# Performance work log

Hardware: AMD Instinct MI355X
Metric: run time of the kernel (lower is better)

## Reference

```python
import jax, jax.numpy as jnp
import numpy as np

B, S, HID, NH, D = 1, 2048, 4096, 32, 128
ROPE_THETA = 10000.0
EPS = 1e-5


def setup_inputs() -> dict:
    key = jax.random.key(0)
    ks = jax.random.split(key, 10)
    w_scale = 1.0 / np.sqrt(HID)
    return {
        "hidden_states": jax.random.normal(ks[0], (B, S, HID), jnp.float32),
        "position_ids": jnp.broadcast_to(jnp.arange(S, dtype=jnp.int32), (B, S)),
        "Wq": jax.random.normal(ks[1], (HID, HID), jnp.float32) * w_scale,
        "Wk": jax.random.normal(ks[2], (HID, HID), jnp.float32) * w_scale,
        "Wv": jax.random.normal(ks[3], (HID, HID), jnp.float32) * w_scale,
        "Wo": jax.random.normal(ks[4], (HID, HID), jnp.float32) * w_scale,
        "qn_w": 1.0 + 0.02 * jax.random.normal(ks[5], (1, D), jnp.float32),
        "qn_b": 0.02 * jax.random.normal(ks[6], (1, D), jnp.float32),
        "kn_w": 1.0 + 0.02 * jax.random.normal(ks[7], (1, D), jnp.float32),
        "kn_b": 0.02 * jax.random.normal(ks[8], (1, D), jnp.float32),
    }


def _head_layernorm(x, gamma, beta, n_heads):
    # x: [B, S, n_heads, D]; gamma/beta: [mp=1, D] repeat-interleaved to [n_heads, D]
    mu = jnp.mean(x, axis=-1, keepdims=True)
    var = jnp.mean(jnp.square(x - mu), axis=-1, keepdims=True)
    xn = (x - mu) * jax.lax.rsqrt(var + EPS)
    g = jnp.repeat(gamma, n_heads // gamma.shape[0], axis=0)  # [n_heads, D]
    b = jnp.repeat(beta, n_heads // beta.shape[0], axis=0)
    return xn * g + b


def _rope_cos_sin(position_ids, dim, dtype):
    inv_freq = 1.0 / (ROPE_THETA ** (jnp.arange(0, dim, 2, dtype=jnp.float32) / dim))
    freqs = position_ids.astype(jnp.float32)[..., None] * inv_freq  # [B, S, D/2]
    emb = jnp.concatenate([freqs, freqs], axis=-1)  # [B, S, D]
    # unsqueeze_dim=-2 -> broadcast over heads in BSND layout
    return jnp.cos(emb)[:, :, None, :].astype(dtype), jnp.sin(emb)[:, :, None, :].astype(dtype)


def _rotate_half(x):
    h = x.shape[-1] // 2
    return jnp.concatenate([-x[..., h:], x[..., :h]], axis=-1)


def reference(hidden_states, position_ids, Wq, Wk, Wv, Wo, qn_w, qn_b, kn_w, kn_b):
    b, s, hid = hidden_states.shape
    d = qn_w.shape[-1]
    nh = hid // d
    nkv = nh  # num_key_value_heads == num_heads for Chameleon-7B (groups=1)

    q = (hidden_states @ Wq).reshape(b, s, nh, d)
    k = (hidden_states @ Wk).reshape(b, s, nkv, d)
    v = (hidden_states @ Wv).reshape(b, s, nkv, d)

    q = _head_layernorm(q, qn_w, qn_b, nh)
    k = _head_layernorm(k, kn_w, kn_b, nkv)

    cos, sin = _rope_cos_sin(position_ids, d, q.dtype)
    q = q * cos + _rotate_half(q) * sin
    k = k * cos + _rotate_half(k) * sin

    scale = d ** -0.5
    scores = jnp.einsum("bqhd,bkhd->bhqk", q, k) * scale  # [B, H, S, S]
    causal = jnp.tril(jnp.ones((s, s), dtype=bool))
    scores = jnp.where(causal[None, None], scores, jnp.finfo(scores.dtype).min)
    probs = jax.nn.softmax(scores, axis=-1)
    attn = jnp.einsum("bhqk,bkhd->bqhd", probs, v).reshape(b, s, hid)
    return attn @ Wo
```

## Files before the change

kernel.cpp:

```cpp
#include <hip/hip_runtime.h>

#define S_LEN 2048
#define HID 4096
#define NH 32
#define HD 128
#define QKV_N 12288

typedef __attribute__((ext_vector_type(8))) short bf16x8;
typedef __attribute__((ext_vector_type(4))) float f32x4;

__device__ __forceinline__ unsigned short f2bf(float f) {
    unsigned int u = __float_as_uint(f);
    u += 0x7FFF + ((u >> 16) & 1);
    return (unsigned short)(u >> 16);
}
__device__ __forceinline__ float bf2f(unsigned short h) {
    return __uint_as_float(((unsigned int)h) << 16);
}

typedef __attribute__((address_space(1))) const void gconst_void;
typedef __attribute__((address_space(3))) void lds_void;
__device__ __forceinline__ void gl16(const void* g, void* l) {
    __builtin_amdgcn_global_load_lds((gconst_void*)g, (lds_void*)l, 16, 0, 0);
}

#define VMCNT(n) asm volatile("s_waitcnt vmcnt(" #n ")" ::: "memory")
#define BAR()    do { asm volatile("" ::: "memory"); __builtin_amdgcn_s_barrier(); asm volatile("" ::: "memory"); } while (0)

__global__ __launch_bounds__(256)
void cvt_f32_bf16(const float* __restrict__ in, unsigned short* __restrict__ out, int n8)
{
    int i = blockIdx.x * 256 + threadIdx.x;
    if (i >= n8) return;
    const float4* p = (const float4*)in + (size_t)i * 2;
    float4 a = p[0], b = p[1];
    bf16x8 o;
    o[0] = (short)f2bf(a.x); o[1] = (short)f2bf(a.y); o[2] = (short)f2bf(a.z); o[3] = (short)f2bf(a.w);
    o[4] = (short)f2bf(b.x); o[5] = (short)f2bf(b.y); o[6] = (short)f2bf(b.z); o[7] = (short)f2bf(b.w);
    *((bf16x8*)out + i) = o;
}

struct W3 { const float* w0; const float* w1; const float* w2; };

__global__ __launch_bounds__(256)
void cvt_w_t3(W3 ws3, unsigned short* __restrict__ Wt, int N, int K)
{
    __shared__ unsigned short t[64][72];
    const float* W = blockIdx.z == 0 ? ws3.w0 : (blockIdx.z == 1 ? ws3.w1 : ws3.w2);
    unsigned short* Wto = Wt + (size_t)blockIdx.z * N * K;
    const int tid = threadIdx.x;
    const int n0 = blockIdx.x * 64, k0 = blockIdx.y * 64;
    const int c4 = (tid & 15) * 4;
    const int r  = tid >> 4;
    #pragma unroll
    for (int p = 0; p < 4; ++p) {
        float4 v = *(const float4*)&W[(size_t)(k0 + r + p * 16) * N + n0 + c4];
        ushort4 o;
        o.x = f2bf(v.x); o.y = f2bf(v.y); o.z = f2bf(v.z); o.w = f2bf(v.w);
        *(ushort4*)&t[r + p * 16][c4] = o;
    }
    __syncthreads();
    const int n = tid >> 2;
    const int kq = (tid & 3) * 16;
    unsigned short* dst = &Wto[(size_t)(n0 + n) * K + k0 + kq];
    bf16x8 v0, v1;
    #pragma unroll
    for (int j = 0; j < 8; ++j) v0[j] = (short)t[kq + j][n];
    #pragma unroll
    for (int j = 0; j < 8; ++j) v1[j] = (short)t[kq + 8 + j][n];
    *(bf16x8*)dst = v0;
    *(bf16x8*)(dst + 8) = v1;
}

template<bool SPLIT>
__global__ __launch_bounds__(256)
void v_transpose(const unsigned short* __restrict__ P0, const unsigned short* __restrict__ P1,
                 unsigned short* __restrict__ Vtg)
{
    __shared__ unsigned short t[64][72];
    const int tid = threadIdx.x;
    const int s0 = blockIdx.x * 64;
    const int c0 = blockIdx.y * 64;
    #pragma unroll
    for (int i = 0; i < 2; ++i) {
        int idx = i * 256 + tid;
        int r = idx >> 3, c8 = (idx & 7) * 8;
        size_t off = (size_t)(s0 + r) * QKV_N + 2 * HID + c0 + c8;
        bf16x8 a = *(const bf16x8*)&P0[off];
        if (SPLIT) {
            bf16x8 b = *(const bf16x8*)&P1[off];
            #pragma unroll
            for (int j = 0; j < 8; ++j)
                a[j] = (short)f2bf(bf2f((unsigned short)a[j]) + bf2f((unsigned short)b[j]));
        }
        *(bf16x8*)&t[r][c8] = a;
    }
    __syncthreads();
    #pragma unroll
    for (int i = 0; i < 2; ++i) {
        int idx = i * 256 + tid;
        int oc = idx >> 3, os8 = (idx & 7) * 8;
        bf16x8 v;
        #pragma unroll
        for (int j = 0; j < 8; ++j) v[j] = (short)t[os8 + j][oc];
        *(bf16x8*)&Vtg[(size_t)(c0 + oc) * S_LEN + s0 + os8] = v;
    }
}

__device__ __forceinline__ void lda4(bf16x8 af[4][2], const char* base, int rq, int l15, int lg) {
    const int sw = (l15 & 7) << 4;
    #pragma unroll
    for (int i = 0; i < 4; ++i) {
        const char* rb = base + ((rq * 4 + i) * 16 + l15) * 128;
        af[i][0] = *(const bf16x8*)(rb + ((lg * 16) ^ sw));
        af[i][1] = *(const bf16x8*)(rb + ((64 + lg * 16) ^ sw));
    }
}
__device__ __forceinline__ void ldb2(bf16x8 bf[2][2], const char* base, int cq, int l15, int lg) {
    const int sw = (l15 & 7) << 4;
    #pragma unroll
    for (int j = 0; j < 2; ++j) {
        const char* rb = base + ((cq * 2 + j) * 16 + l15) * 128;
        bf[j][0] = *(const bf16x8*)(rb + ((lg * 16) ^ sw));
        bf[j][1] = *(const bf16x8*)(rb + ((64 + lg * 16) ^ sw));
    }
}
__device__ __forceinline__ void mfma16(f32x4 acc[8][4], const bf16x8 af[4][2], const bf16x8 bf[2][2],
                                       int mi0, int nj0) {
    __builtin_amdgcn_s_setprio(1);
    #pragma unroll
    for (int kk = 0; kk < 2; ++kk)
        #pragma unroll
        for (int i = 0; i < 4; ++i)
            #pragma unroll
            for (int j = 0; j < 2; ++j)
                acc[mi0 + i][nj0 + j] =
                    __builtin_amdgcn_mfma_f32_16x16x32_bf16(af[i][kk], bf[j][kk], acc[mi0 + i][nj0 + j], 0, 0, 0);
    __builtin_amdgcn_s_setprio(0);
}
__device__ __forceinline__ void stage2(const unsigned short* g, char* dst, int ldk, int r32, int kn) {
    gl16(g + (size_t)r32 * ldk + kn, dst);
    gl16(g + (size_t)(r32 + 8) * ldk + kn, dst + 1024);
}

__global__ __launch_bounds__(512, 2)
void gemm256(const unsigned short* __restrict__ A,
             const unsigned short* __restrict__ Bt,
             unsigned short* __restrict__ Cp,
             int N, int K, int ldk, size_t zstride)
{
    extern __shared__ char lds[];
    const int tid = threadIdx.x;
    const int l   = tid & 63;
    const int l15 = l & 15, lg = l >> 4;
    const int wid = tid >> 6;
    const int wr  = wid >> 2;
    const int wc  = wid & 3;

    const int nwg = gridDim.x;
    const int bid = blockIdx.x;
    const int ntx = N >> 8;
    const int nty = nwg / ntx;
    const int cpx = ntx >> 3;
    const int xcd = bid & 7;
    const int idx = bid >> 3;
    const int bx = xcd * cpx + idx / nty;
    const int by = idx % nty;
    const int m0 = by * 256, n0 = bx * 256;
    const int koff = blockIdx.z * K;

    char* const Abase = lds + wr * 16384;
    char* const Bbase = lds + 32768 + (wc >> 1) * 16384 + (wc & 1) * 8192;

    const int l8 = l >> 3, l7 = l & 7;
    const int swslot = (l7 ^ l8) << 3;

    const unsigned short* Ag = A  + (size_t)(m0 + wr * 128 + wc * 16 + l8) * ldk + koff + swslot;
    const unsigned short* Bg = Bt + (size_t)(n0 + wc * 64 + wr * 16 + l8) * ldk + koff + swslot;
    char* const Adst = Abase + (wc * 16) * 128 + l * 16;
    char* const Bdst = Bbase + (wr * 16) * 128 + l * 16;

    f32x4 acc[8][4] = {};
    bf16x8 af[4][2], bfA[2][2], bfB[2][2];

    stage2(Ag, Adst, ldk, 0, 0);
    stage2(Bg, Bdst, ldk, 0, 0);
    stage2(Ag, Adst + 64 * 128, ldk, 64, 0);
    stage2(Bg, Bdst + 32 * 128, ldk, 32, 0);
    VMCNT(0);
    BAR();

    const int NT = K >> 6;
    for (int t = 0; t < NT; ++t) {
        const int cb = (t & 1) * 65536, nb = cb ^ 65536;
        const int kn = (t + 1) << 6;
        const bool hn = (t + 1) < NT;

        lda4(af, Abase + cb, 0, l15, lg);
        ldb2(bfA, Bbase + cb, 0, l15, lg);
        if (hn) {
            stage2(Ag, Adst + nb, ldk, 0, kn);
            stage2(Bg, Bdst + nb, ldk, 0, kn);
            stage2(Ag, Adst + nb + 64 * 128, ldk, 64, kn);
            stage2(Bg, Bdst + nb + 32 * 128, ldk, 32, kn);
        }
        mfma16(acc, af, bfA, 0, 0);

        ldb2(bfB, Bbase + cb, 1, l15, lg);
        mfma16(acc, af, bfB, 0, 2);

        lda4(af, Abase + cb, 1, l15, lg);
        mfma16(acc, af, bfB, 4, 2);
        mfma16(acc, af, bfA, 4, 0);

        VMCNT(0);
        BAR();
    }

    unsigned short* C = Cp + (size_t)blockIdx.z * zstride;
    const int crow = m0 + wr * 128 + lg * 4;
    const int ccol = n0 + wc * 64 + l15;
    #pragma unroll
    for (int mi = 0; mi < 8; ++mi)
        #pragma unroll
        for (int nj = 0; nj < 4; ++nj)
            #pragma unroll
            for (int rr = 0; rr < 4; ++rr)
                C[(size_t)(crow + mi * 16 + rr) * N + ccol + nj * 16] = f2bf(acc[mi][nj][rr]);
}

__global__ __launch_bounds__(256)
void combine2(const unsigned short* __restrict__ P, float* __restrict__ out)
{
    const size_t i = ((size_t)blockIdx.x * 256 + threadIdx.x) * 8;
    const size_t stride = (size_t)S_LEN * HID;
    bf16x8 a = *(const bf16x8*)&P[i];
    bf16x8 b = *(const bf16x8*)&P[stride + i];
    #pragma unroll
    for (int j = 0; j < 8; ++j)
        out[i + j] = bf2f((unsigned short)a[j]) + bf2f((unsigned short)b[j]);
}

template<bool SPLIT>
__global__ __launch_bounds__(256)
void ln_rope(unsigned short* __restrict__ P0, const unsigned short* __restrict__ P1,
             const float* __restrict__ qg, const float* __restrict__ qb,
             const float* __restrict__ kg, const float* __restrict__ kb,
             const int* __restrict__ pos)
{
    const int tid = threadIdx.x;
    const int l = tid & 63;
    const int w = tid >> 6;
    const int rid = blockIdx.x * 4 + w;
    const int s = rid >> 6;
    const int hh = rid & 63;
    const int which = hh >> 5;
    const int h = hh & 31;
    const size_t off = (size_t)s * QKV_N + which * HID + h * HD;
    unsigned short* p = P0 + off;
    const float* gamma = which ? kg : qg;
    const float* beta  = which ? kb : qb;

    float lo = bf2f(p[l]);
    float hi = bf2f(p[l + 64]);
    if (SPLIT) {
        const unsigned short* q = P1 + off;
        lo += bf2f(q[l]);
        hi += bf2f(q[l + 64]);
    }
    float sum = lo + hi;
    #pragma unroll
    for (int off2 = 32; off2 >= 1; off2 >>= 1) sum += __shfl_xor(sum, off2, 64);
    float mu = sum * (1.0f / 128.0f);
    float dlo = lo - mu, dhi = hi - mu;
    float vs = dlo * dlo + dhi * dhi;
    #pragma unroll
    for (int off2 = 32; off2 >= 1; off2 >>= 1) vs += __shfl_xor(vs, off2, 64);
    float rstd = rsqrtf(vs * (1.0f / 128.0f) + 1e-5f);
    float xlo = dlo * rstd * gamma[l] + beta[l];
    float xhi = dhi * rstd * gamma[l + 64] + beta[l + 64];

    float fpos = (float)pos[s];
    float invf = exp2f(-13.287712379549449f * (float)l * (1.0f / 64.0f));
    float ang = fpos * invf;
    float sn, cs;
    sincosf(ang, &sn, &cs);
    p[l]      = f2bf(xlo * cs - xhi * sn);
    p[l + 64] = f2bf(xhi * cs + xlo * sn);
}

#define KVB 128
#define ATTN_LDS 149504

__global__ __launch_bounds__(512)
void attn_fwd(const unsigned short* __restrict__ QKV,
              const unsigned short* __restrict__ Vtg,
              unsigned short* __restrict__ O)
{
    extern __shared__ char shb[];
    unsigned short* const Psw = (unsigned short*)(shb + 131072) + (threadIdx.x >> 6) * (16 * 72);

    const int tid = threadIdx.x;
    const int l = tid & 63;
    const int w = tid >> 6;
    const int l15 = l & 15, lg = l >> 4;
    const int h = blockIdx.y;
    const int qb = gridDim.x - 1 - blockIdx.x;
    const int q0 = qb * 128;
    const int qw = q0 + w * 16;

    const unsigned short* Qp = QKV + h * HD;
    const unsigned short* Kp = QKV + HID + h * HD;
    const unsigned short* Vp = Vtg + (size_t)h * HD * S_LEN;

    bf16x8 qf[4];
    #pragma unroll
    for (int d = 0; d < 4; ++d)
        qf[d] = *(const bf16x8*)&Qp[(size_t)(qw + l15) * QKV_N + d * 32 + lg * 8];

    f32x4 o_acc[8] = {};
    float mgrp = -1e30f;
    float lsum[4] = {0.0f, 0.0f, 0.0f, 0.0f};

    const float scale = 0.08838834764831845f;

    const int ksl = tid & 15;
    const int kr7 = (tid >> 4) & 7;
    const int ksg = (ksl & 8) | ((ksl ^ kr7) & 7);
    const unsigned short* Kg = Kp + (size_t)(tid >> 4) * QKV_N + ksg * 8;
    const unsigned short* Vg = Vp + (size_t)(tid >> 4) * S_LEN + ksg * 8;

#define STAGE(buf, kv0s) do {                                                          \
    _Pragma("unroll")                                                                  \
    for (int i_ = 0; i_ < 4; ++i_)                                                     \
        gl16(Kg + (size_t)((kv0s) + i_ * 32) * QKV_N,                                  \
             shb + (buf) * 32768 + (i_ * 512 + tid) * 16);                             \
    _Pragma("unroll")                                                                  \
    for (int i_ = 0; i_ < 4; ++i_)                                                     \
        gl16(Vg + (size_t)i_ * 32 * S_LEN + (kv0s),                                    \
             shb + 65536 + (buf) * 32768 + (i_ * 512 + tid) * 16);                     \
} while (0)

    STAGE(0, 0);
    VMCNT(0);
    __syncthreads();

    const int nt = qb + 1;
    for (int t = 0; t < nt; ++t) {
        const int kv0 = t * KVB;
        const int cur = t & 1;
        const bool hn = (t + 1) < nt;
        if (hn) STAGE(cur ^ 1, kv0 + KVB);

        f32x4 sc[8] = {};
        const char* Kb = shb + cur * 32768;
        #pragma unroll
        for (int kvf = 0; kvf < 8; ++kvf) {
            int r = kvf * 16 + l15;
            int sw = (r & 7) << 4;
            #pragma unroll
            for (int d = 0; d < 4; ++d) {
                bf16x8 kf = *(const bf16x8*)(Kb + r * 256 + ((d * 64 + lg * 16) ^ sw));
                sc[kvf] = __builtin_amdgcn_mfma_f32_16x16x32_bf16(qf[d], kf, sc[kvf], 0, 0, 0);
            }
        }

        const bool full = (kv0 + KVB <= qw);
        if (!full) {
            #pragma unroll
            for (int k = 0; k < 8; ++k) {
                #pragma unroll
                for (int r = 0; r < 4; ++r) {
                    int qg = qw + lg * 4 + r;
                    if (kv0 + k * 16 + l15 > qg) sc[k][r] = -1e30f;
                }
            }
        }
        float mx = fmaxf(fmaxf(sc[0][0], sc[0][1]), fmaxf(sc[0][2], sc[0][3]));
        #pragma unroll
        for (int k = 1; k < 8; ++k) {
            float m2 = fmaxf(fmaxf(sc[k][0], sc[k][1]), fmaxf(sc[k][2], sc[k][3]));
            mx = fmaxf(mx, m2);
        }
        mx *= scale;
        #pragma unroll
        for (int off = 8; off >= 1; off >>= 1) mx = fmaxf(mx, __shfl_xor(mx, off, 64));
        if (!__all(mx <= mgrp + 8.0f)) {
            float mn = fmaxf(mgrp, mx);
            float corr = __expf(mgrp - mn);
            #pragma unroll
            for (int r = 0; r < 4; ++r) lsum[r] *= corr;
            #pragma unroll
            for (int df = 0; df < 8; ++df) o_acc[df] *= corr;
            mgrp = mn;
        }
        const float mn = mgrp;

        float ph[4][4];
        #pragma unroll
        for (int r = 0; r < 4; ++r) {
            int ql = lg * 4 + r;
            float psum = 0.0f;
            #pragma unroll
            for (int k = 0; k < 8; ++k) {
                float p = __expf(fmaf(sc[k][r], scale, -mn));
                psum += p;
                if (k < 4) Psw[ql * 72 + k * 16 + l15] = f2bf(p);
                else       ph[r][k - 4] = p;
            }
            lsum[r] += psum;
        }

        const char* Vb = shb + 65536 + cur * 32768;
        {
            bf16x8 pa0 = *(const bf16x8*)&Psw[l15 * 72 + lg * 8];
            bf16x8 pa1 = *(const bf16x8*)&Psw[l15 * 72 + 32 + lg * 8];
            #pragma unroll
            for (int df = 0; df < 8; ++df) {
                int d = df * 16 + l15;
                int sw = (d & 7) << 4;
                const char* vrow = Vb + d * 256;
                bf16x8 v0 = *(const bf16x8*)(vrow + ((lg * 16) ^ sw));
                bf16x8 v1 = *(const bf16x8*)(vrow + ((64 + lg * 16) ^ sw));
                o_acc[df] = __builtin_amdgcn_mfma_f32_16x16x32_bf16(pa0, v0, o_acc[df], 0, 0, 0);
                o_acc[df] = __builtin_amdgcn_mfma_f32_16x16x32_bf16(pa1, v1, o_acc[df], 0, 0, 0);
            }
        }
        #pragma unroll
        for (int r = 0; r < 4; ++r) {
            int ql = lg * 4 + r;
            #pragma unroll
            for (int k = 0; k < 4; ++k)
                Psw[ql * 72 + k * 16 + l15] = f2bf(ph[r][k]);
        }
        {
            bf16x8 pa0 = *(const bf16x8*)&Psw[l15 * 72 + lg * 8];
            bf16x8 pa1 = *(const bf16x8*)&Psw[l15 * 72 + 32 + lg * 8];
            #pragma unroll
            for (int df = 0; df < 8; ++df) {
                int d = df * 16 + l15;
                int sw = (d & 7) << 4;
                const char* vrow = Vb + d * 256;
                bf16x8 v0 = *(const bf16x8*)(vrow + ((128 + lg * 16) ^ sw));
                bf16x8 v1 = *(const bf16x8*)(vrow + ((128 + 64 + lg * 16) ^ sw));
                o_acc[df] = __builtin_amdgcn_mfma_f32_16x16x32_bf16(pa0, v0, o_acc[df], 0, 0, 0);
                o_acc[df] = __builtin_amdgcn_mfma_f32_16x16x32_bf16(pa1, v1, o_acc[df], 0, 0, 0);
            }
        }

        if (hn) {
            VMCNT(0);
            BAR();
        }
    }
#undef STAGE

    float inv[4];
    #pragma unroll
    for (int r = 0; r < 4; ++r) {
        float s = lsum[r];
        #pragma unroll
        for (int off = 8; off >= 1; off >>= 1) s += __shfl_xor(s, off, 64);
        inv[r] = 1.0f / s;
    }
    #pragma unroll
    for (int df = 0; df < 8; ++df) {
        #pragma unroll
        for (int r = 0; r < 4; ++r) {
            int q = qw + lg * 4 + r;
            int d = h * HD + df * 16 + l15;
            O[(size_t)q * HID + d] = f2bf(o_acc[df][r] * inv[r]);
        }
    }
}

extern "C" void kernel_launch(void* const* d_in, const int* in_sizes, int n_in,
                              void* d_out, int out_size, void* d_ws, size_t ws_size,
                              hipStream_t stream)
{
    (void)in_sizes; (void)n_in; (void)out_size;
    const float* X    = (const float*)d_in[0];
    const int*   pos  = (const int*)d_in[1];
    const float* Wq   = (const float*)d_in[2];
    const float* Wk   = (const float*)d_in[3];
    const float* Wv   = (const float*)d_in[4];
    const float* Wo   = (const float*)d_in[5];
    const float* qn_w = (const float*)d_in[6];
    const float* qn_b = (const float*)d_in[7];
    const float* kn_w = (const float*)d_in[8];
    const float* kn_b = (const float*)d_in[9];
    float* out = (float*)d_out;

    unsigned short* Xb    = (unsigned short*)d_ws;
    unsigned short* QKVb  = (unsigned short*)((char*)d_ws + 16777216);
    unsigned short* Wt    = (unsigned short*)((char*)d_ws + 67108864);
    unsigned short* Pp    = (unsigned short*)((char*)d_ws + 100663296);
    unsigned short* Vtg   = (unsigned short*)((char*)d_ws + 134217728);
    unsigned short* P1    = (unsigned short*)((char*)d_ws + 167772160);
    unsigned short* Ab    = Xb;

    const bool splitQKV = ws_size >= (size_t)218103808;

    (void)hipFuncSetAttribute((const void*)gemm256, hipFuncAttributeMaxDynamicSharedMemorySize, 131072);
    (void)hipFuncSetAttribute((const void*)attn_fwd, hipFuncAttributeMaxDynamicSharedMemorySize, ATTN_LDS);

    dim3 blk(256);

    cvt_f32_bf16<<<dim3((S_LEN * HID / 8 + 255) / 256), blk, 0, stream>>>(X, Xb, S_LEN * HID / 8);

    W3 w3{Wq, Wk, Wv};
    cvt_w_t3<<<dim3(HID / 64, HID / 64, 3), blk, 0, stream>>>(w3, Wt, HID, HID);

    if (splitQKV) {
        gemm256<<<dim3(384, 1, 2), dim3(512), 131072, stream>>>(
            Xb, Wt, QKVb, QKV_N, HID / 2, HID, (size_t)75497472);
        v_transpose<true><<<dim3(S_LEN / 64, HID / 64), blk, 0, stream>>>(QKVb, P1, Vtg);
        ln_rope<true><<<dim3(S_LEN * 64 / 4), blk, 0, stream>>>(QKVb, P1, qn_w, qn_b, kn_w, kn_b, pos);
    } else {
        gemm256<<<dim3(384, 1, 1), dim3(512), 131072, stream>>>(
            Xb, Wt, QKVb, QKV_N, HID, HID, (size_t)0);
        v_transpose<false><<<dim3(S_LEN / 64, HID / 64), blk, 0, stream>>>(QKVb, QKVb, Vtg);
        ln_rope<false><<<dim3(S_LEN * 64 / 4), blk, 0, stream>>>(QKVb, QKVb, qn_w, qn_b, kn_w, kn_b, pos);
    }

    attn_fwd<<<dim3(S_LEN / 128, NH), dim3(512), ATTN_LDS, stream>>>(QKVb, Vtg, Ab);

    W3 wo3{Wo, Wo, Wo};
    cvt_w_t3<<<dim3(HID / 64, HID / 64, 1), blk, 0, stream>>>(wo3, Wt, HID, HID);

    gemm256<<<dim3(128, 1, 2), dim3(512), 131072, stream>>>(
        Ab, Wt, Pp, HID, HID / 2, HID, (size_t)S_LEN * HID);
    combine2<<<dim3(S_LEN * HID / 8 / 256), blk, 0, stream>>>(Pp, out);
}
```

Before: 484.0 us.

## Replace split-K output GEMM and combine with single 128x256-tile GEMM writing fp32

The output projection used a split-K 256x256-tile GEMM that wrote two bf16 partial buffers, followed by a combine kernel that summed them into fp32. It now runs a dedicated GEMM with 128x256 tiles over the full K, launching 256 blocks with two blocks per CU and writing fp32 directly. This removes the partial-buffer traffic, the extra kernel launch, and the bf16 rounding of partials. The trade-off is a longer K loop per block and smaller tiles with less reuse, in exchange for better CU fill without split-K.

```diff
diff --git a/kernel.cpp b/kernel.cpp
--- a/kernel.cpp
+++ b/kernel.cpp
@@ -229,16 +229,97 @@
                 C[(size_t)(crow + mi * 16 + rr) * N + ccol + nj * 16] = f2bf(acc[mi][nj][rr]);
 }
 
-__global__ __launch_bounds__(256)
-void combine2(const unsigned short* __restrict__ P, float* __restrict__ out)
-{
-    const size_t i = ((size_t)blockIdx.x * 256 + threadIdx.x) * 8;
-    const size_t stride = (size_t)S_LEN * HID;
-    bf16x8 a = *(const bf16x8*)&P[i];
-    bf16x8 b = *(const bf16x8*)&P[stride + i];
-    #pragma unroll
-    for (int j = 0; j < 8; ++j)
-        out[i + j] = bf2f((unsigned short)a[j]) + bf2f((unsigned short)b[j]);
+__global__ __launch_bounds__(512, 2)
+void gemm_wo(const unsigned short* __restrict__ A,
+             const unsigned short* __restrict__ Bt,
+             float* __restrict__ out, int N, int K)
+{
+    extern __shared__ char lds[];
+    const int tid = threadIdx.x;
+    const int l   = tid & 63;
+    const int l15 = l & 15, lg = l >> 4;
+    const int wid = tid >> 6;
+    const int wr  = wid >> 2;
+    const int wc  = wid & 3;
+
+    const int bid = blockIdx.x;
+    const int ntx = N >> 8;
+    const int nty = 256 / ntx;
+    const int cpx = ntx >> 3;
+    const int xcd = bid & 7;
+    const int idx = bid >> 3;
+    const int bx = xcd * cpx + idx / nty;
+    const int by = idx % nty;
+    const int m0 = by * 128, n0 = bx * 256;
+
+    const int r8 = tid >> 3;
+    const int swslot = ((tid & 7) ^ (r8 & 7)) << 3;
+
+    const unsigned short* Ag = A  + (size_t)(m0 + r8) * K + swslot;
+    const unsigned short* Bg = Bt + (size_t)(n0 + r8) * K + swslot;
+
+    f32x4 acc[4][4] = {};
+    bf16x8 af[4][2], bf[4][2];
+
+    #pragma unroll
+    for (int i = 0; i < 2; ++i)
+        gl16(Ag + (size_t)i * 64 * K, lds + (i * 512 + tid) * 16);
+    #pragma unroll
+    for (int i = 0; i < 4; ++i)
+        gl16(Bg + (size_t)i * 64 * K, lds + 16384 + (i * 512 + tid) * 16);
+    VMCNT(0);
+    BAR();
+
+    const int NT = K >> 6;
+    for (int t = 0; t < NT; ++t) {
+        const int cb = (t & 1) * 49152, nb = cb ^ 49152;
+        const int kn = (t + 1) << 6;
+        const bool hn = (t + 1) < NT;
+
+        const int sw = (l15 & 7) << 4;
+        #pragma unroll
+        for (int mi = 0; mi < 4; ++mi) {
+            const char* rb = lds + cb + (wr * 64 + mi * 16 + l15) * 128;
+            af[mi][0] = *(const bf16x8*)(rb + ((lg * 16) ^ sw));
+            af[mi][1] = *(const bf16x8*)(rb + ((64 + lg * 16) ^ sw));
+        }
+        #pragma unroll
+        for (int nj = 0; nj < 4; ++nj) {
+            const char* rb = lds + cb + 16384 + (wc * 64 + nj * 16 + l15) * 128;
+            bf[nj][0] = *(const bf16x8*)(rb + ((lg * 16) ^ sw));
+            bf[nj][1] = *(const bf16x8*)(rb + ((64 + lg * 16) ^ sw));
+        }
+        if (hn) {
+            #pragma unroll
+            for (int i = 0; i < 2; ++i)
+                gl16(Ag + (size_t)i * 64 * K + kn, lds + nb + (i * 512 + tid) * 16);
+            #pragma unroll
+            for (int i = 0; i < 4; ++i)
+                gl16(Bg + (size_t)i * 64 * K + kn, lds + nb + 16384 + (i * 512 + tid) * 16);
+        }
+        __builtin_amdgcn_s_setprio(1);
+        #pragma unroll
+        for (int kk = 0; kk < 2; ++kk)
+            #pragma unroll
+            for (int mi = 0; mi < 4; ++mi)
+                #pragma unroll
+                for (int nj = 0; nj < 4; ++nj)
+                    acc[mi][nj] = __builtin_amdgcn_mfma_f32_16x16x32_bf16(af[mi][kk], bf[nj][kk], acc[mi][nj], 0, 0, 0);
+        __builtin_amdgcn_s_setprio(0);
+
+        VMCNT(0);
+        BAR();
+    }
+
+    const int crow = m0 + wr * 64 + lg * 4;
+    const int ccol = n0 + wc * 64 + l15;
+    #pragma unroll
+    for (int mi = 0; mi < 4; ++mi)
+        #pragma unroll
+        for (int nj = 0; nj < 4; ++nj)
+            #pragma unroll
+            for (int rr = 0; rr < 4; ++rr)
+                out[(size_t)(crow + mi * 16 + rr) * N + ccol + nj * 16] = acc[mi][nj][rr];
 }
 
 template<bool SPLIT>
@@ -494,7 +575,6 @@
     unsigned short* Xb    = (unsigned short*)d_ws;
     unsigned short* QKVb  = (unsigned short*)((char*)d_ws + 16777216);
     unsigned short* Wt    = (unsigned short*)((char*)d_ws + 67108864);
-    unsigned short* Pp    = (unsigned short*)((char*)d_ws + 100663296);
     unsigned short* Vtg   = (unsigned short*)((char*)d_ws + 134217728);
     unsigned short* P1    = (unsigned short*)((char*)d_ws + 167772160);
     unsigned short* Ab    = Xb;
@@ -502,6 +582,7 @@
     const bool splitQKV = ws_size >= (size_t)218103808;
 
     (void)hipFuncSetAttribute((const void*)gemm256, hipFuncAttributeMaxDynamicSharedMemorySize, 131072);
+    (void)hipFuncSetAttribute((const void*)gemm_wo, hipFuncAttributeMaxDynamicSharedMemorySize, 98304);
     (void)hipFuncSetAttribute((const void*)attn_fwd, hipFuncAttributeMaxDynamicSharedMemorySize, ATTN_LDS);
 
     dim3 blk(256);
@@ -528,7 +609,5 @@
     W3 wo3{Wo, Wo, Wo};
     cvt_w_t3<<<dim3(HID / 64, HID / 64, 1), blk, 0, stream>>>(wo3, Wt, HID, HID);
 
-    gemm256<<<dim3(128, 1, 2), dim3(512), 131072, stream>>>(
-        Ab, Wt, Pp, HID, HID / 2, HID, (size_t)S_LEN * HID);
-    combine2<<<dim3(S_LEN * HID / 8 / 256), blk, 0, stream>>>(Pp, out);
-}
+    gemm_wo<<<dim3(256), dim3(512), 98304, stream>>>(Ab, Wt, out, HID, HID);
+}
```

Result: no change. 475.4 us, median of 3 (-1.8%).
